# Optimization experiments

Measured on AMD Instinct MI355X. Metric: run time of the kernel, lower is better.

Reference implementation:

```python
import jax, jax.numpy as jnp
import numpy as np

MARGIN = 1.0
ALFA = 0.1


def setup_inputs() -> dict:
    key = jax.random.key(0)
    k1, k2 = jax.random.split(key)
    N, D, T = 262144, 128, 262144
    embeddings = jax.random.normal(k1, (N, D), dtype=jnp.float32)
    triplets = jax.random.randint(k2, (T, 3), 0, N, dtype=jnp.int64)
    return {"embeddings": embeddings, "triplets": triplets}


def _corr_loss(embeddings):
    # torch_cov(rowvar=False): columns are variables -> D x D covariance
    N, D = embeddings.shape
    m = embeddings - jnp.mean(embeddings, axis=0, keepdims=True)  # [N, D]
    cov = jnp.einsum('ni,nj->ij', m, m) / (N - 1)                 # [D, D]
    V = jnp.diagonal(cov)                                          # variances
    corr2 = (cov / jnp.sqrt(V[:, None] * V[None, :])) ** 2
    # strict lower triangle, n*(n-1)/2 elements, then mean
    tril = jnp.tril(jnp.ones((D, D), dtype=corr2.dtype), k=-1)
    return jnp.sum(corr2 * tril) / (D * (D - 1) / 2)


def _triplet_loss(embeddings, triplets):
    pivot = embeddings[triplets[:, 0]]
    positives = embeddings[triplets[:, 1]]
    negatives = embeddings[triplets[:, 2]]
    ap = jnp.sum((pivot - positives) ** 2, axis=1)
    an = jnp.sum((pivot - negatives) ** 2, axis=1)
    return jnp.mean(jax.nn.relu(ap - an + MARGIN))


def reference(embeddings, triplets):
    corr_loss = _corr_loss(embeddings)
    triplet_loss = _triplet_loss(embeddings, triplets)
    return triplet_loss + ALFA * corr_loss
```

## Files before the change

kernel.cpp:

```cpp
#include <hip/hip_runtime.h>

#define D 128
#define MARGIN 1.0f
#define ALFA 0.1f
#define KC 64
#define GB 512
#define TBLK 1024

#define WS_TSUM   0
#define WS_GRAM   256
#define WS_COLSUM (WS_GRAM + D * D)
#define WS_ZERO   (WS_COLSUM + D)
#define WS_PART   16896
#define PART_STRIDE (D * D + D)

typedef __attribute__((ext_vector_type(8)))  short bf16x8;
typedef __attribute__((ext_vector_type(16))) float f32x16;

__device__ __forceinline__ unsigned short f2bf(float f) {
    unsigned u = __float_as_uint(f);
    u += 0x7FFFu + ((u >> 16) & 1u);
    return (unsigned short)(u >> 16);
}

__device__ __forceinline__ float d2diff(float4 p, float4 q, float4 r) {
    float ax = p.x - q.x, ay = p.y - q.y, az = p.z - q.z, aw = p.w - q.w;
    float bx = p.x - r.x, by = p.y - r.y, bz = p.z - r.z, bw = p.w - r.w;
    return (ax * ax + ay * ay + az * az + aw * aw)
         - (bx * bx + by * by + bz * bz + bw * bw);
}

template<bool ATOMIC>
__global__ __launch_bounds__(512, 4) void fused_kernel(const float* __restrict__ emb,
                                                       const int* __restrict__ trip,
                                                       int rowsPerBlock, int T,
                                                       float* __restrict__ ws) {
    __shared__ __align__(16) char lds[2][128 * 128];
    __shared__ float csred[D];

    const int tid = threadIdx.x;

    if (blockIdx.x < GB) {
        const int l   = tid & 63;
        const int w   = tid >> 6;
        const int r0  = blockIdx.x * rowsPerBlock;

        const int rT = w & 3;
        const int c0 = (w >> 2) * 2;

        f32x16 acc0 = {};
        f32x16 acc1 = {};
        float cs[4] = {0.f, 0.f, 0.f, 0.f};
        const int d0 = (tid & 31) * 4;

        auto stage = [&](int cc, int b) {
#pragma unroll
            for (int j = 0; j < 2; ++j) {
                const int k = j * 32 + (tid >> 5) * 2;
                const float* base = emb + (size_t)(r0 + cc * KC + k) * D + d0;
                float4 a  = *(const float4*)base;
                float4 bv = *(const float4*)(base + D);
#pragma unroll
                for (int i = 0; i < 4; ++i) {
                    float av = ((const float*)&a)[i];
                    float bb = ((const float*)&bv)[i];
                    cs[i] += av + bb;
                    unsigned slotp = (unsigned)(k >> 3) ^ (unsigned)((tid & 31) & 7);
                    unsigned off = (unsigned)(d0 + i) * 128u + slotp * 16u + (unsigned)((k & 7) << 1);
                    *(unsigned*)(&lds[b][off]) = (unsigned)f2bf(av) | ((unsigned)f2bf(bb) << 16);
                }
            }
        };

        auto frag = [&](int t, int kb, int b) -> bf16x8 {
            const int d = t * 32 + (l & 31);
            const int k = kb + (l >> 5) * 8;
            unsigned slotp = (unsigned)(k >> 3) ^ ((unsigned)(d >> 2) & 7u);
            return *(const bf16x8*)(&lds[b][(unsigned)d * 128u + slotp * 16u]);
        };

        const int nChunks = rowsPerBlock / KC;
        stage(0, 0);
        for (int cc = 0; cc < nChunks; ++cc) {
            const int b = cc & 1;
            __syncthreads();
            if (cc + 1 < nChunks) stage(cc + 1, b ^ 1);
#pragma unroll
            for (int kb = 0; kb < KC; kb += 16) {
                bf16x8 fr = frag(rT,     kb, b);
                bf16x8 f0 = frag(c0,     kb, b);
                bf16x8 f1 = frag(c0 + 1, kb, b);
                acc0 = __builtin_amdgcn_mfma_f32_32x32x16_bf16(fr, f0, acc0, 0, 0, 0);
                acc1 = __builtin_amdgcn_mfma_f32_32x32x16_bf16(fr, f1, acc1, 0, 0, 0);
            }
        }
        __syncthreads();

        if (tid < D) csred[tid] = 0.f;
        __syncthreads();
#pragma unroll
        for (int i = 0; i < 4; ++i) atomicAdd(&csred[d0 + i], cs[i]);
        __syncthreads();

        float* gram   = ATOMIC ? ws + WS_GRAM
                               : ws + WS_PART + (size_t)blockIdx.x * PART_STRIDE;
        float* colsum = ATOMIC ? ws + WS_COLSUM : gram + D * D;

        if (tid < D) {
            if (ATOMIC) atomicAdd(&colsum[tid], csred[tid]);
            else        colsum[tid] = csred[tid];
        }

        const int row_hi = (l >> 5) * 4;
        const int col    = l & 31;
#pragma unroll
        for (int reg = 0; reg < 16; ++reg) {
            const int row32 = (reg & 3) + 8 * (reg >> 2) + row_hi;
            const int gr    = (rT * 32 + row32) * D;
            if (ATOMIC) {
                atomicAdd(&gram[gr + c0 * 32 + col],       acc0[reg]);
                atomicAdd(&gram[gr + (c0 + 1) * 32 + col], acc1[reg]);
            } else {
                gram[gr + c0 * 32 + col]       = acc0[reg];
                gram[gr + (c0 + 1) * 32 + col] = acc1[reg];
            }
        }
    } else {
        const int li  = tid & 31;
        const int hwl = tid >> 5;
        const int hw  = (blockIdx.x - GB) * 16 + hwl;
        const int NH  = TBLK * 16;

        float wsum = 0.f;

        for (int t0 = hw; t0 < T; t0 += 4 * NH) {
            float4 P[4], Q[4], R[4];
#pragma unroll
            for (int k = 0; k < 4; ++k) {
                const int t = t0 + k * NH;
                if (t < T) {
                    const int i0 = trip[3 * t], i1 = trip[3 * t + 1], i2 = trip[3 * t + 2];
                    P[k] = ((const float4*)(emb + (size_t)i0 * D))[li];
                    Q[k] = ((const float4*)(emb + (size_t)i1 * D))[li];
                    R[k] = ((const float4*)(emb + (size_t)i2 * D))[li];
                }
            }
#pragma unroll
            for (int k = 0; k < 4; ++k) {
                const int t = t0 + k * NH;
                if (t < T) {
                    float s = d2diff(P[k], Q[k], R[k]);
#pragma unroll
                    for (int off = 16; off; off >>= 1) s += __shfl_xor(s, off, 64);
                    if (li == 0) wsum += fmaxf(s + MARGIN, 0.f);
                }
            }
        }

        if (li == 0) csred[hwl] = wsum;
        __syncthreads();
        if (tid == 0) {
            float b = 0.f;
#pragma unroll
            for (int i = 0; i < 16; ++i) b += csred[i];
            atomicAdd(&ws[WS_TSUM], b);
        }
    }
}

__global__ __launch_bounds__(256) void reduce_partials(float* __restrict__ ws, int P, int slices) {
    const int nIdxBlocks = (PART_STRIDE + 255) / 256;
    const int idx   = (blockIdx.x % nIdxBlocks) * 256 + threadIdx.x;
    const int slice = blockIdx.x / nIdxBlocks;
    if (idx >= PART_STRIDE) return;
    const int per = P / slices;
    const float* part = ws + WS_PART;
    float s = 0.f;
    const int p0 = slice * per;
#pragma unroll 8
    for (int p = 0; p < per; ++p)
        s += part[(size_t)(p0 + p) * PART_STRIDE + idx];
    if (idx < D * D) atomicAdd(&ws[WS_GRAM + idx], s);
    else             atomicAdd(&ws[WS_COLSUM + (idx - D * D)], s);
}

__global__ __launch_bounds__(256) void finalize_kernel(const float* __restrict__ ws,
                                                       float* __restrict__ out,
                                                       int N, int T) {
    const float* gram   = ws + WS_GRAM;
    const float* colsum = ws + WS_COLSUM;

    __shared__ float V[D];
    __shared__ float red[256];

    const int tid = threadIdx.x;
    const float invN   = 1.0f / (float)N;
    const float invNm1 = 1.0f / (float)(N - 1);

    if (tid < D) {
        float m = colsum[tid] * invN;
        V[tid] = (gram[tid * D + tid] - (float)N * m * m) * invNm1;
    }
    __syncthreads();

    float local = 0.f;
    for (int idx = tid; idx < D * D; idx += 256) {
        int i = idx >> 7, j = idx & 127;
        if (j < i) {
            float mi  = colsum[i] * invN;
            float mj  = colsum[j] * invN;
            float cov = (gram[idx] - (float)N * mi * mj) * invNm1;
            local += cov * cov / (V[i] * V[j]);
        }
    }
    red[tid] = local;
    __syncthreads();
    for (int s = 128; s > 0; s >>= 1) {
        if (tid < s) red[tid] += red[tid + s];
        __syncthreads();
    }
    if (tid == 0) {
        float corr_mean = red[0] / ((float)D * (float)(D - 1) * 0.5f);
        out[0] = ws[WS_TSUM] / (float)T + ALFA * corr_mean;
    }
}

extern "C" void kernel_launch(void* const* d_in, const int* in_sizes, int n_in,
                              void* d_out, int out_size, void* d_ws, size_t ws_size,
                              hipStream_t stream) {
    const float* emb  = (const float*)d_in[0];
    const int*   trip = (const int*)d_in[1];
    float*       out  = (float*)d_out;
    float*       ws   = (float*)d_ws;

    const int N = in_sizes[0] / D;
    const int T = in_sizes[1] / 3;

    hipMemsetAsync(d_ws, 0, WS_ZERO * sizeof(float), stream);

    const size_t needP = ((size_t)WS_PART + (size_t)GB * PART_STRIDE) * sizeof(float);

    if (ws_size >= needP) {
        fused_kernel<false><<<GB + TBLK, 512, 0, stream>>>(emb, trip, N / GB, T, ws);
        reduce_partials<<<65 * 16, 256, 0, stream>>>(ws, GB, 16);
    } else {
        fused_kernel<true><<<GB + TBLK, 512, 0, stream>>>(emb, trip, N / GB, T, ws);
    }

    finalize_kernel<<<1, 256, 0, stream>>>(ws, out, N, T);
}
```

Before: 275.3 us.

## Write bf16 embedding table in gram kernel and gather triplets from it

The gram kernel now also stores a bf16 copy of the embeddings to workspace while staging, and a separate triplet kernel gathers the pivot, positive and negative rows from this half-size table. This halves the bytes moved by the random-access triplet gather and makes the table small enough to stay cache-resident. In exchange it adds a 64MB write, serializes the triplet pass after the gram pass instead of overlapping them in one fused launch, and reduces triplet distance precision to bf16 inputs. The old fused kernel is kept as a fallback when workspace is too small.

```diff
diff --git a/kernel.cpp b/kernel.cpp
--- a/kernel.cpp
+++ b/kernel.cpp
@@ -5,7 +5,6 @@
 #define ALFA 0.1f
 #define KC 64
 #define GB 512
-#define TBLK 1024
 
 #define WS_TSUM   0
 #define WS_GRAM   256
@@ -13,8 +12,10 @@
 #define WS_ZERO   (WS_COLSUM + D)
 #define WS_PART   16896
 #define PART_STRIDE (D * D + D)
+#define WS_TAB_F  (WS_PART + GB * PART_STRIDE)
 
 typedef __attribute__((ext_vector_type(8)))  short bf16x8;
+typedef __attribute__((ext_vector_type(8)))  unsigned short u16x8;
 typedef __attribute__((ext_vector_type(16))) float f32x16;
 
 __device__ __forceinline__ unsigned short f2bf(float f) {
@@ -22,149 +23,153 @@
     u += 0x7FFFu + ((u >> 16) & 1u);
     return (unsigned short)(u >> 16);
 }
-
-__device__ __forceinline__ float d2diff(float4 p, float4 q, float4 r) {
-    float ax = p.x - q.x, ay = p.y - q.y, az = p.z - q.z, aw = p.w - q.w;
-    float bx = p.x - r.x, by = p.y - r.y, bz = p.z - r.z, bw = p.w - r.w;
-    return (ax * ax + ay * ay + az * az + aw * aw)
-         - (bx * bx + by * by + bz * bz + bw * bw);
-}
-
-template<bool ATOMIC>
-__global__ __launch_bounds__(512, 4) void fused_kernel(const float* __restrict__ emb,
-                                                       const int* __restrict__ trip,
-                                                       int rowsPerBlock, int T,
-                                                       float* __restrict__ ws) {
+__device__ __forceinline__ float bf2f(unsigned short u) {
+    return __uint_as_float((unsigned)u << 16);
+}
+
+__global__ __launch_bounds__(512, 4) void gram_mfma_write(const float* __restrict__ emb,
+                                                          int rowsPerBlock,
+                                                          float* __restrict__ ws,
+                                                          unsigned short* __restrict__ tab) {
     __shared__ __align__(16) char lds[2][128 * 128];
     __shared__ float csred[D];
 
     const int tid = threadIdx.x;
-
-    if (blockIdx.x < GB) {
-        const int l   = tid & 63;
-        const int w   = tid >> 6;
-        const int r0  = blockIdx.x * rowsPerBlock;
-
-        const int rT = w & 3;
-        const int c0 = (w >> 2) * 2;
-
-        f32x16 acc0 = {};
-        f32x16 acc1 = {};
-        float cs[4] = {0.f, 0.f, 0.f, 0.f};
-        const int d0 = (tid & 31) * 4;
-
-        auto stage = [&](int cc, int b) {
-#pragma unroll
-            for (int j = 0; j < 2; ++j) {
-                const int k = j * 32 + (tid >> 5) * 2;
-                const float* base = emb + (size_t)(r0 + cc * KC + k) * D + d0;
-                float4 a  = *(const float4*)base;
-                float4 bv = *(const float4*)(base + D);
-#pragma unroll
-                for (int i = 0; i < 4; ++i) {
-                    float av = ((const float*)&a)[i];
-                    float bb = ((const float*)&bv)[i];
-                    cs[i] += av + bb;
-                    unsigned slotp = (unsigned)(k >> 3) ^ (unsigned)((tid & 31) & 7);
-                    unsigned off = (unsigned)(d0 + i) * 128u + slotp * 16u + (unsigned)((k & 7) << 1);
-                    *(unsigned*)(&lds[b][off]) = (unsigned)f2bf(av) | ((unsigned)f2bf(bb) << 16);
+    const int l   = tid & 63;
+    const int w   = tid >> 6;
+    const int r0  = blockIdx.x * rowsPerBlock;
+
+    const int rT = w & 3;
+    const int c0 = (w >> 2) * 2;
+
+    f32x16 acc0 = {};
+    f32x16 acc1 = {};
+    float cs[4] = {0.f, 0.f, 0.f, 0.f};
+    const int d0 = (tid & 31) * 4;
+
+    auto stage = [&](int cc, int b) {
+#pragma unroll
+        for (int j = 0; j < 2; ++j) {
+            const int k = j * 32 + (tid >> 5) * 2;
+            const int rowg = r0 + cc * KC + k;
+            const float* base = emb + (size_t)rowg * D + d0;
+            float4 a  = *(const float4*)base;
+            float4 bv = *(const float4*)(base + D);
+            ushort4 ua, ub;
+            unsigned short* pa = (unsigned short*)&ua;
+            unsigned short* pb = (unsigned short*)&ub;
+#pragma unroll
+            for (int i = 0; i < 4; ++i) {
+                float av = ((const float*)&a)[i];
+                float bb = ((const float*)&bv)[i];
+                cs[i] += av + bb;
+                unsigned short ha = f2bf(av), hb = f2bf(bb);
+                pa[i] = ha; pb[i] = hb;
+                unsigned slotp = (unsigned)(k >> 3) ^ (unsigned)((tid & 31) & 7);
+                unsigned off = (unsigned)(d0 + i) * 128u + slotp * 16u + (unsigned)((k & 7) << 1);
+                *(unsigned*)(&lds[b][off]) = (unsigned)ha | ((unsigned)hb << 16);
+            }
+            *(ushort4*)&tab[(size_t)rowg * D + d0]       = ua;
+            *(ushort4*)&tab[(size_t)(rowg + 1) * D + d0] = ub;
+        }
+    };
+
+    auto frag = [&](int t, int kb, int b) -> bf16x8 {
+        const int d = t * 32 + (l & 31);
+        const int k = kb + (l >> 5) * 8;
+        unsigned slotp = (unsigned)(k >> 3) ^ ((unsigned)(d >> 2) & 7u);
+        return *(const bf16x8*)(&lds[b][(unsigned)d * 128u + slotp * 16u]);
+    };
+
+    const int nChunks = rowsPerBlock / KC;
+    stage(0, 0);
+    for (int cc = 0; cc < nChunks; ++cc) {
+        const int b = cc & 1;
+        __syncthreads();
+        if (cc + 1 < nChunks) stage(cc + 1, b ^ 1);
+#pragma unroll
+        for (int kb = 0; kb < KC; kb += 16) {
+            bf16x8 fr = frag(rT,     kb, b);
+            bf16x8 f0 = frag(c0,     kb, b);
+            bf16x8 f1 = frag(c0 + 1, kb, b);
+            acc0 = __builtin_amdgcn_mfma_f32_32x32x16_bf16(fr, f0, acc0, 0, 0, 0);
+            acc1 = __builtin_amdgcn_mfma_f32_32x32x16_bf16(fr, f1, acc1, 0, 0, 0);
+        }
+    }
+    __syncthreads();
+
+    if (tid < D) csred[tid] = 0.f;
+    __syncthreads();
+#pragma unroll
+    for (int i = 0; i < 4; ++i) atomicAdd(&csred[d0 + i], cs[i]);
+    __syncthreads();
+
+    float* gram   = ws + WS_PART + (size_t)blockIdx.x * PART_STRIDE;
+    float* colsum = gram + D * D;
+
+    if (tid < D) colsum[tid] = csred[tid];
+
+    const int row_hi = (l >> 5) * 4;
+    const int col    = l & 31;
+#pragma unroll
+    for (int reg = 0; reg < 16; ++reg) {
+        const int row32 = (reg & 3) + 8 * (reg >> 2) + row_hi;
+        const int gr    = (rT * 32 + row32) * D;
+        gram[gr + c0 * 32 + col]       = acc0[reg];
+        gram[gr + (c0 + 1) * 32 + col] = acc1[reg];
+    }
+}
+
+__global__ __launch_bounds__(256) void triplet_bf16(const unsigned short* __restrict__ tab,
+                                                    const int* __restrict__ trip,
+                                                    int T,
+                                                    float* __restrict__ ws) {
+    const int tid = threadIdx.x;
+    const int li  = tid & 15;
+    const int grp = (blockIdx.x * 256 + tid) >> 4;
+    const int NG  = (gridDim.x * 256) >> 4;
+
+    float wsum = 0.f;
+
+    for (int t0 = grp; t0 < T; t0 += 4 * NG) {
+        u16x8 P[4], Q[4], R[4];
+#pragma unroll
+        for (int u = 0; u < 4; ++u) {
+            const int t = t0 + u * NG;
+            if (t < T) {
+                const int i0 = trip[3 * t], i1 = trip[3 * t + 1], i2 = trip[3 * t + 2];
+                P[u] = *(const u16x8*)&tab[(size_t)i0 * D + li * 8];
+                Q[u] = *(const u16x8*)&tab[(size_t)i1 * D + li * 8];
+                R[u] = *(const u16x8*)&tab[(size_t)i2 * D + li * 8];
+            }
+        }
+#pragma unroll
+        for (int u = 0; u < 4; ++u) {
+            const int t = t0 + u * NG;
+            if (t < T) {
+                float s = 0.f;
+#pragma unroll
+                for (int e = 0; e < 8; ++e) {
+                    float p = bf2f(P[u][e]);
+                    float dp = p - bf2f(Q[u][e]);
+                    float dn = p - bf2f(R[u][e]);
+                    s += dp * dp - dn * dn;
                 }
-            }
-        };
-
-        auto frag = [&](int t, int kb, int b) -> bf16x8 {
-            const int d = t * 32 + (l & 31);
-            const int k = kb + (l >> 5) * 8;
-            unsigned slotp = (unsigned)(k >> 3) ^ ((unsigned)(d >> 2) & 7u);
-            return *(const bf16x8*)(&lds[b][(unsigned)d * 128u + slotp * 16u]);
-        };
-
-        const int nChunks = rowsPerBlock / KC;
-        stage(0, 0);
-        for (int cc = 0; cc < nChunks; ++cc) {
-            const int b = cc & 1;
-            __syncthreads();
-            if (cc + 1 < nChunks) stage(cc + 1, b ^ 1);
-#pragma unroll
-            for (int kb = 0; kb < KC; kb += 16) {
-                bf16x8 fr = frag(rT,     kb, b);
-                bf16x8 f0 = frag(c0,     kb, b);
-                bf16x8 f1 = frag(c0 + 1, kb, b);
-                acc0 = __builtin_amdgcn_mfma_f32_32x32x16_bf16(fr, f0, acc0, 0, 0, 0);
-                acc1 = __builtin_amdgcn_mfma_f32_32x32x16_bf16(fr, f1, acc1, 0, 0, 0);
-            }
-        }
-        __syncthreads();
-
-        if (tid < D) csred[tid] = 0.f;
-        __syncthreads();
-#pragma unroll
-        for (int i = 0; i < 4; ++i) atomicAdd(&csred[d0 + i], cs[i]);
-        __syncthreads();
-
-        float* gram   = ATOMIC ? ws + WS_GRAM
-                               : ws + WS_PART + (size_t)blockIdx.x * PART_STRIDE;
-        float* colsum = ATOMIC ? ws + WS_COLSUM : gram + D * D;
-
-        if (tid < D) {
-            if (ATOMIC) atomicAdd(&colsum[tid], csred[tid]);
-            else        colsum[tid] = csred[tid];
-        }
-
-        const int row_hi = (l >> 5) * 4;
-        const int col    = l & 31;
-#pragma unroll
-        for (int reg = 0; reg < 16; ++reg) {
-            const int row32 = (reg & 3) + 8 * (reg >> 2) + row_hi;
-            const int gr    = (rT * 32 + row32) * D;
-            if (ATOMIC) {
-                atomicAdd(&gram[gr + c0 * 32 + col],       acc0[reg]);
-                atomicAdd(&gram[gr + (c0 + 1) * 32 + col], acc1[reg]);
-            } else {
-                gram[gr + c0 * 32 + col]       = acc0[reg];
-                gram[gr + (c0 + 1) * 32 + col] = acc1[reg];
-            }
-        }
-    } else {
-        const int li  = tid & 31;
-        const int hwl = tid >> 5;
-        const int hw  = (blockIdx.x - GB) * 16 + hwl;
-        const int NH  = TBLK * 16;
-
-        float wsum = 0.f;
-
-        for (int t0 = hw; t0 < T; t0 += 4 * NH) {
-            float4 P[4], Q[4], R[4];
-#pragma unroll
-            for (int k = 0; k < 4; ++k) {
-                const int t = t0 + k * NH;
-                if (t < T) {
-                    const int i0 = trip[3 * t], i1 = trip[3 * t + 1], i2 = trip[3 * t + 2];
-                    P[k] = ((const float4*)(emb + (size_t)i0 * D))[li];
-                    Q[k] = ((const float4*)(emb + (size_t)i1 * D))[li];
-                    R[k] = ((const float4*)(emb + (size_t)i2 * D))[li];
-                }
-            }
-#pragma unroll
-            for (int k = 0; k < 4; ++k) {
-                const int t = t0 + k * NH;
-                if (t < T) {
-                    float s = d2diff(P[k], Q[k], R[k]);
-#pragma unroll
-                    for (int off = 16; off; off >>= 1) s += __shfl_xor(s, off, 64);
-                    if (li == 0) wsum += fmaxf(s + MARGIN, 0.f);
-                }
-            }
-        }
-
-        if (li == 0) csred[hwl] = wsum;
-        __syncthreads();
-        if (tid == 0) {
-            float b = 0.f;
-#pragma unroll
-            for (int i = 0; i < 16; ++i) b += csred[i];
-            atomicAdd(&ws[WS_TSUM], b);
-        }
+#pragma unroll
+                for (int off = 8; off; off >>= 1) s += __shfl_xor(s, off, 64);
+                if (li == 0) wsum += fmaxf(s + MARGIN, 0.f);
+            }
+        }
+    }
+
+    __shared__ float red[16];
+    if (li == 0) red[tid >> 4] = wsum;
+    __syncthreads();
+    if (tid == 0) {
+        float b = 0.f;
+#pragma unroll
+        for (int i = 0; i < 16; ++i) b += red[i];
+        atomicAdd(&ws[WS_TSUM], b);
     }
 }
 
@@ -225,6 +230,120 @@
     }
 }
 
+__device__ __forceinline__ float d2diff(float4 p, float4 q, float4 r) {
+    float ax = p.x - q.x, ay = p.y - q.y, az = p.z - q.z, aw = p.w - q.w;
+    float bx = p.x - r.x, by = p.y - r.y, bz = p.z - r.z, bw = p.w - r.w;
+    return (ax * ax + ay * ay + az * az + aw * aw)
+         - (bx * bx + by * by + bz * bz + bw * bw);
+}
+
+__global__ __launch_bounds__(512, 4) void fused_fallback(const float* __restrict__ emb,
+                                                         const int* __restrict__ trip,
+                                                         int rowsPerBlock, int T,
+                                                         float* __restrict__ ws) {
+    __shared__ __align__(16) char lds[2][128 * 128];
+    __shared__ float csred[D];
+    const int tid = threadIdx.x;
+
+    if (blockIdx.x < GB) {
+        const int l = tid & 63, w = tid >> 6, r0 = blockIdx.x * rowsPerBlock;
+        const int rT = w & 3, c0 = (w >> 2) * 2;
+        f32x16 acc0 = {}, acc1 = {};
+        float cs[4] = {0.f, 0.f, 0.f, 0.f};
+        const int d0 = (tid & 31) * 4;
+
+        auto stage = [&](int cc, int b) {
+#pragma unroll
+            for (int j = 0; j < 2; ++j) {
+                const int k = j * 32 + (tid >> 5) * 2;
+                const float* base = emb + (size_t)(r0 + cc * KC + k) * D + d0;
+                float4 a = *(const float4*)base;
+                float4 bv = *(const float4*)(base + D);
+#pragma unroll
+                for (int i = 0; i < 4; ++i) {
+                    float av = ((const float*)&a)[i], bb = ((const float*)&bv)[i];
+                    cs[i] += av + bb;
+                    unsigned slotp = (unsigned)(k >> 3) ^ (unsigned)((tid & 31) & 7);
+                    unsigned off = (unsigned)(d0 + i) * 128u + slotp * 16u + (unsigned)((k & 7) << 1);
+                    *(unsigned*)(&lds[b][off]) = (unsigned)f2bf(av) | ((unsigned)f2bf(bb) << 16);
+                }
+            }
+        };
+        auto frag = [&](int t, int kb, int b) -> bf16x8 {
+            const int d = t * 32 + (l & 31);
+            const int k = kb + (l >> 5) * 8;
+            unsigned slotp = (unsigned)(k >> 3) ^ ((unsigned)(d >> 2) & 7u);
+            return *(const bf16x8*)(&lds[b][(unsigned)d * 128u + slotp * 16u]);
+        };
+        const int nChunks = rowsPerBlock / KC;
+        stage(0, 0);
+        for (int cc = 0; cc < nChunks; ++cc) {
+            const int b = cc & 1;
+            __syncthreads();
+            if (cc + 1 < nChunks) stage(cc + 1, b ^ 1);
+#pragma unroll
+            for (int kb = 0; kb < KC; kb += 16) {
+                bf16x8 fr = frag(rT, kb, b);
+                bf16x8 f0 = frag(c0, kb, b);
+                bf16x8 f1 = frag(c0 + 1, kb, b);
+                acc0 = __builtin_amdgcn_mfma_f32_32x32x16_bf16(fr, f0, acc0, 0, 0, 0);
+                acc1 = __builtin_amdgcn_mfma_f32_32x32x16_bf16(fr, f1, acc1, 0, 0, 0);
+            }
+        }
+        __syncthreads();
+        if (tid < D) csred[tid] = 0.f;
+        __syncthreads();
+#pragma unroll
+        for (int i = 0; i < 4; ++i) atomicAdd(&csred[d0 + i], cs[i]);
+        __syncthreads();
+        if (tid < D) atomicAdd(&ws[WS_COLSUM + tid], csred[tid]);
+        const int row_hi = (l >> 5) * 4, col = l & 31;
+#pragma unroll
+        for (int reg = 0; reg < 16; ++reg) {
+            const int row32 = (reg & 3) + 8 * (reg >> 2) + row_hi;
+            const int gr = (rT * 32 + row32) * D;
+            atomicAdd(&ws[WS_GRAM + gr + c0 * 32 + col], acc0[reg]);
+            atomicAdd(&ws[WS_GRAM + gr + (c0 + 1) * 32 + col], acc1[reg]);
+        }
+    } else {
+        const int li = tid & 31, hwl = tid >> 5;
+        const int hw = (blockIdx.x - GB) * 16 + hwl;
+        const int NH = 1024 * 16;
+        float wsum = 0.f;
+        for (int t0 = hw; t0 < T; t0 += 4 * NH) {
+            float4 P[4], Q[4], R[4];
+#pragma unroll
+            for (int k = 0; k < 4; ++k) {
+                const int t = t0 + k * NH;
+                if (t < T) {
+                    const int i0 = trip[3 * t], i1 = trip[3 * t + 1], i2 = trip[3 * t + 2];
+                    P[k] = ((const float4*)(emb + (size_t)i0 * D))[li];
+                    Q[k] = ((const float4*)(emb + (size_t)i1 * D))[li];
+                    R[k] = ((const float4*)(emb + (size_t)i2 * D))[li];
+                }
+            }
+#pragma unroll
+            for (int k = 0; k < 4; ++k) {
+                const int t = t0 + k * NH;
+                if (t < T) {
+                    float s = d2diff(P[k], Q[k], R[k]);
+#pragma unroll
+                    for (int off = 16; off; off >>= 1) s += __shfl_xor(s, off, 64);
+                    if (li == 0) wsum += fmaxf(s + MARGIN, 0.f);
+                }
+            }
+        }
+        if (li == 0) csred[hwl] = wsum;
+        __syncthreads();
+        if (tid == 0) {
+            float b = 0.f;
+#pragma unroll
+            for (int i = 0; i < 16; ++i) b += csred[i];
+            atomicAdd(&ws[WS_TSUM], b);
+        }
+    }
+}
+
 extern "C" void kernel_launch(void* const* d_in, const int* in_sizes, int n_in,
                               void* d_out, int out_size, void* d_ws, size_t ws_size,
                               hipStream_t stream) {
@@ -238,13 +357,15 @@
 
     hipMemsetAsync(d_ws, 0, WS_ZERO * sizeof(float), stream);
 
-    const size_t needP = ((size_t)WS_PART + (size_t)GB * PART_STRIDE) * sizeof(float);
-
-    if (ws_size >= needP) {
-        fused_kernel<false><<<GB + TBLK, 512, 0, stream>>>(emb, trip, N / GB, T, ws);
+    const size_t needB = (size_t)WS_TAB_F * 4 + (size_t)N * D * 2;
+
+    if (ws_size >= needB) {
+        unsigned short* tab = (unsigned short*)(ws + WS_TAB_F);
+        gram_mfma_write<<<GB, 512, 0, stream>>>(emb, N / GB, ws, tab);
+        triplet_bf16<<<1024, 256, 0, stream>>>(tab, trip, T, ws);
         reduce_partials<<<65 * 16, 256, 0, stream>>>(ws, GB, 16);
     } else {
-        fused_kernel<true><<<GB + TBLK, 512, 0, stream>>>(emb, trip, N / GB, T, ws);
+        fused_fallback<<<GB + 1024, 512, 0, stream>>>(emb, trip, N / GB, T, ws);
     }
 
     finalize_kernel<<<1, 256, 0, stream>>>(ws, out, N, T);
```

After: 276.9 us. Within noise of the previous version (+0.6%).
